# Kernel optimization log

Hardware: AMD Instinct MI355X
Metric: run time of the kernel (lower is better)

## Reference

```python
import jax, jax.numpy as jnp
import numpy as np


def _gcn(x, src, dst, W, b, n):
    # symmetric normalization: deg computed on edges WITH self-loops (weights 1)
    deg = jax.ops.segment_sum(jnp.ones_like(src, dtype=x.dtype), dst, num_segments=n)
    dinv = jnp.where(deg > 0, jax.lax.rsqrt(deg), 0.0)
    norm = dinv[src] * dinv[dst]              # [E+n]
    xw = x @ W                                # [n, out] transform first (cheaper)
    msg = xw[src] * norm[:, None]             # gather + edge scale
    return jax.ops.segment_sum(msg, dst, num_segments=n) + b


def setup_inputs() -> dict:
    key = jax.random.key(0)
    ks = jax.random.split(key, 8)
    N, E = 100_000, 1_280_000
    x = jax.random.normal(ks[0], (N, 18), dtype=jnp.float32)
    edge_index = jax.random.randint(ks[1], (2, E), 0, N, dtype=jnp.int32)
    W1 = jax.random.normal(ks[2], (18, 32), dtype=jnp.float32) * 0.2
    b1 = jnp.zeros((32,), dtype=jnp.float32)
    W2 = jax.random.normal(ks[3], (32, 64), dtype=jnp.float32) * 0.15
    b2 = jnp.zeros((64,), dtype=jnp.float32)
    Wfc = jax.random.normal(ks[4], (64, 2), dtype=jnp.float32) * 0.1
    bfc = jnp.zeros((2,), dtype=jnp.float32)
    return {"x": x, "edge_index": edge_index, "W1": W1, "b1": b1,
            "W2": W2, "b2": b2, "Wfc": Wfc, "bfc": bfc}


def reference(x, edge_index, W1, b1, W2, b2, Wfc, bfc):
    n = x.shape[0]
    loop = jnp.arange(n, dtype=edge_index.dtype)
    src = jnp.concatenate([edge_index[0], loop])   # add self-loops (PyG default)
    dst = jnp.concatenate([edge_index[1], loop])
    h = jax.nn.relu(_gcn(x, src, dst, W1, b1, n))
    h = jax.nn.relu(_gcn(h, src, dst, W2, b2, n))
    logits = h @ Wfc + bfc
    return jax.nn.log_softmax(logits, axis=1)
```

## Files before the change

kernel.cpp:

```cpp
#include <hip/hip_runtime.h>
#include <hip/hip_fp16.h>
#include <math.h>


#define TPB 256
#define BSH 8
#define BNODES 256
#define MAXBUCK 512
#define CH 8192
#define NPW 8
#define CAPSH 13
#define CAP (1 << CAPSH)

__global__ void k_part(const int* __restrict__ src, const int* __restrict__ dst,
                       int* __restrict__ bcursor, int* __restrict__ eb,
                       __half* __restrict__ u1h, __half* __restrict__ u2h,
                       int E, int n, int nbuck) {
    __shared__ int lh[MAXBUCK];
    __shared__ int lbase[MAXBUCK];
    int t = threadIdx.x;
    if (blockIdx.x == 0 && t < 32) {
        u1h[(size_t)n * 32 + t] = __float2half_rn(0.f);
        u2h[(size_t)n * 32 + t] = __float2half_rn(0.f);
    }
    int chunk0 = blockIdx.x * CH;
    int end = min(chunk0 + CH, E);
    const int4* dst4 = (const int4*)dst;
    const int4* src4 = (const int4*)src;
    for (int i = t; i < nbuck; i += TPB) lh[i] = 0;
    __syncthreads();
    for (int e4 = chunk0 / 4 + t; e4 * 4 < end; e4 += TPB) {
        int base = e4 * 4;
        int4 d = dst4[e4];
        if (base + 0 < end) atomicAdd(&lh[d.x >> BSH], 1);
        if (base + 1 < end) atomicAdd(&lh[d.y >> BSH], 1);
        if (base + 2 < end) atomicAdd(&lh[d.z >> BSH], 1);
        if (base + 3 < end) atomicAdd(&lh[d.w >> BSH], 1);
    }
    __syncthreads();
    for (int i = t; i < nbuck; i += TPB) {
        int c = lh[i];
        lbase[i] = c ? atomicAdd(&bcursor[i], c) : 0;
        lh[i] = 0;
    }
    __syncthreads();
    for (int e4 = chunk0 / 4 + t; e4 * 4 < end; e4 += TPB) {
        int base = e4 * 4;
        int4 d = dst4[e4];
        int4 s = src4[e4];
        #define PUT(c, sv) if (base + c < end) { \
            int b = (d.sv) >> BSH; \
            int r = lbase[b] + atomicAdd(&lh[b], 1); \
            if (r < CAP) \
                eb[((size_t)b << CAPSH) + r] = ((s.sv) << BSH) | ((d.sv) & (BNODES - 1)); }
        PUT(0, x) PUT(1, y) PUT(2, z) PUT(3, w)
        #undef PUT
    }
}

__global__ void k_bucket(const int* __restrict__ eb, const int* __restrict__ bcursor,
                         const float* __restrict__ x,
                         int* __restrict__ csr, int* __restrict__ row_start,
                         int* __restrict__ cnt4, float* __restrict__ dinv,
                         __half* __restrict__ u1h, int n) {
    __shared__ int lcnt[BNODES];
    __shared__ int lscan[BNODES];
    __shared__ float ldinv[BNODES];
    int b = blockIdx.x;
    int t = threadIdx.x;
    int node0 = b << BSH;
    int beg = b << CAPSH;
    int end = beg + min(bcursor[b], CAP);
    lcnt[t] = 0;
    __syncthreads();
    for (int i = beg + t; i < end; i += TPB)
        atomicAdd(&lcnt[eb[i] & (BNODES - 1)], 1);
    __syncthreads();
    int v = lcnt[t];
    int pad = (v + 3) & ~3;
    lscan[t] = pad;
    __syncthreads();
    for (int off = 1; off < TPB; off <<= 1) {
        int xx = (t >= off) ? lscan[t - off] : 0;
        __syncthreads();
        lscan[t] += xx;
        __syncthreads();
    }
    int pexcl = lscan[t] - pad;
    int node = node0 + t;
    float dv = rsqrtf(1.0f + (float)v);
    ldinv[t] = dv;
    if (node < n) {
        row_start[node] = beg + pexcl;
        cnt4[node] = pad >> 2;
        dinv[node] = dv;
    }
    __syncthreads();
    lcnt[t] = pexcl;
    __syncthreads();
    for (int i = beg + t; i < end; i += TPB) {
        int e = eb[i];
        int p = atomicAdd(&lcnt[e & (BNODES - 1)], 1);
        csr[beg + p] = e >> BSH;
    }
    __syncthreads();
    for (int p = v; p < pad; ++p) csr[beg + pexcl + p] = n;
    int nn = min(BNODES, n - node0);
    int tot = nn * 32;
    const float* xb = x + (size_t)node0 * 18;
    __half* ub = u1h + (size_t)node0 * 32;
    for (int i = t; i < tot; i += TPB) {
        int nl = i >> 5, f = i & 31;
        float val = (f < 18) ? xb[nl * 18 + f] * ldinv[nl] : 0.f;
        ub[i] = __float2half_rn(val);
    }
}

template <int OS, int NW>
__global__ void k_agg(const __half2* __restrict__ uh2, const int* __restrict__ row_start,
                      const int* __restrict__ cnt4, const int* __restrict__ csr,
                      float* __restrict__ agg, int n) {
    int t = blockIdx.x * blockDim.x + threadIdx.x;
    int node = t >> 4, f2 = t & 15;
    if (node >= n) return;
    int beg = row_start[node];
    int it = cnt4[node];
    float2 acc = __half22float2(uh2[(size_t)node * 16 + f2]);
    const int4* ip = (const int4*)(csr + beg);
    for (int i = 0; i < it; ++i) {
        int4 s = ip[i];
        float2 v0 = __half22float2(uh2[(size_t)s.x * 16 + f2]);
        float2 v1 = __half22float2(uh2[(size_t)s.y * 16 + f2]);
        float2 v2 = __half22float2(uh2[(size_t)s.z * 16 + f2]);
        float2 v3 = __half22float2(uh2[(size_t)s.w * 16 + f2]);
        acc.x += (v0.x + v1.x) + (v2.x + v3.x);
        acc.y += (v0.y + v1.y) + (v2.y + v3.y);
    }
    if (f2 < NW) *(float2*)(agg + (size_t)node * OS + 2 * f2) = acc;
}

__global__ void k_l1(const float* __restrict__ agg1, const float* __restrict__ W1,
                     const float* __restrict__ dinv, const float* __restrict__ b1,
                     __half* __restrict__ u2h, int n) {
    int lane = threadIdx.x & 63;
    int f = lane & 31;
    int wid = __builtin_amdgcn_readfirstlane((int)(threadIdx.x >> 6));
    int wave = blockIdx.x * (TPB / 64) + wid;
    float w1r[18];
#pragma unroll
    for (int k = 0; k < 18; ++k) w1r[k] = W1[k * 32 + f];
    float b1v = b1[f];
    int node0 = wave * NPW;
    for (int r = 0; r < NPW; ++r) {
        int node = node0 + r;
        if (node >= n) return;
        const float* rp = agg1 + (size_t)node * 18;
        float a = 0.f;
#pragma unroll
        for (int k = 0; k < 18; ++k) a = fmaf(rp[k], w1r[k], a);
        float di = dinv[node];
        if (lane < 32)
            u2h[(size_t)node * 32 + f] =
                __float2half_rn(fmaxf(fmaf(di, a, b1v), 0.f) * di);
    }
}

__global__ void k_l2_out(const float* __restrict__ agg2, const float* __restrict__ W2,
                         const float* __restrict__ dinv, const float* __restrict__ b2,
                         const float* __restrict__ Wfc, const float* __restrict__ bfc,
                         float* __restrict__ out, int n) {
    int lane = threadIdx.x & 63;
    int wid = __builtin_amdgcn_readfirstlane((int)(threadIdx.x >> 6));
    int wave = blockIdx.x * (TPB / 64) + wid;
    float w2r[32];
#pragma unroll
    for (int k = 0; k < 32; ++k) w2r[k] = W2[k * 64 + lane];
    float b2v = b2[lane];
    float wf0 = Wfc[lane * 2 + 0], wf1 = Wfc[lane * 2 + 1];
    float bf0 = bfc[0], bf1 = bfc[1];
    int node0 = wave * NPW;
    for (int r = 0; r < NPW; ++r) {
        int node = node0 + r;
        if (node >= n) return;
        const float* rp = agg2 + (size_t)node * 32;
        float a0 = 0.f, a1 = 0.f, a2 = 0.f, a3 = 0.f;
#pragma unroll
        for (int k = 0; k < 32; k += 4) {
            a0 = fmaf(rp[k],     w2r[k],     a0);
            a1 = fmaf(rp[k + 1], w2r[k + 1], a1);
            a2 = fmaf(rp[k + 2], w2r[k + 2], a2);
            a3 = fmaf(rp[k + 3], w2r[k + 3], a3);
        }
        float a = (a0 + a1) + (a2 + a3);
        float v = fmaxf(fmaf(dinv[node], a, b2v), 0.f);
        float l0 = v * wf0;
        float l1 = v * wf1;
#pragma unroll
        for (int off = 32; off >= 1; off >>= 1) {
            l0 += __shfl_xor(l0, off, 64);
            l1 += __shfl_xor(l1, off, 64);
        }
        if (lane == 0) {
            l0 += bf0;
            l1 += bf1;
            float m2 = fmaxf(l0, l1);
            float lse = m2 + logf(expf(l0 - m2) + expf(l1 - m2));
            out[node * 2 + 0] = l0 - lse;
            out[node * 2 + 1] = l1 - lse;
        }
    }
}

extern "C" void kernel_launch(void* const* d_in, const int* in_sizes, int n_in,
                              void* d_out, int out_size, void* d_ws, size_t ws_size,
                              hipStream_t stream) {
    const float* x   = (const float*)d_in[0];
    const int*   ei  = (const int*)d_in[1];
    const float* W1  = (const float*)d_in[2];
    const float* b1  = (const float*)d_in[3];
    const float* W2  = (const float*)d_in[4];
    const float* b2  = (const float*)d_in[5];
    const float* Wfc = (const float*)d_in[6];
    const float* bfc = (const float*)d_in[7];
    float* out = (float*)d_out;

    const int n = in_sizes[0] / 18;
    const int E = in_sizes[1] / 2;
    const int* src = ei;
    const int* dst = ei + E;
    const int nbuck = (n + BNODES - 1) >> BSH;

    char* w = (char*)d_ws;
    int*    bcursor   = (int*)w;     w += (size_t)nbuck * 4;
    int*    row_start = (int*)w;     w += (size_t)n * 4;
    int*    cnt4      = (int*)w;     w += (size_t)n * 4;
    float*  dinv      = (float*)w;   w += (size_t)n * 4;
    int*    eb        = (int*)w;     w += (size_t)nbuck * CAP * 4;
    int*    csr       = (int*)w;     w += (size_t)nbuck * CAP * 4;
    float*  agg1      = (float*)w;   w += (size_t)n * 18 * 4;
    float*  agg2      = (float*)w;   w += (size_t)n * 32 * 4;
    w = (char*)(((size_t)w + 63) & ~(size_t)63);
    __half* u1h       = (__half*)w;  w += (size_t)(n + 1) * 32 * 2;
    w = (char*)(((size_t)w + 63) & ~(size_t)63);
    __half* u2h       = (__half*)w;  w += (size_t)(n + 1) * 32 * 2;

    auto blocks = [](long long work) { return (int)((work + TPB - 1) / TPB); };

    hipMemsetAsync(bcursor, 0, (size_t)nbuck * 4, stream);
    k_part<<<(E + CH - 1) / CH, TPB, 0, stream>>>(src, dst, bcursor, eb, u1h, u2h, E, n, nbuck);
    k_bucket<<<nbuck, TPB, 0, stream>>>(eb, bcursor, x, csr, row_start, cnt4, dinv, u1h, n);

    const int blocksA = blocks((long long)n * 16);
    const int wavesT = (n + NPW - 1) / NPW;
    const int blocksT = (wavesT + (TPB / 64) - 1) / (TPB / 64);

    k_agg<18, 9><<<blocksA, TPB, 0, stream>>>((const __half2*)u1h, row_start, cnt4, csr, agg1, n);
    k_l1<<<blocksT, TPB, 0, stream>>>(agg1, W1, dinv, b1, u2h, n);

    k_agg<32, 16><<<blocksA, TPB, 0, stream>>>((const __half2*)u2h, row_start, cnt4, csr, agg2, n);
    k_l2_out<<<blocksT, TPB, 0, stream>>>(agg2, W2, dinv, b2, Wfc, bfc, out, n);
}
```

Measured before the change: 195.6 us.

## Fuse neighbor aggregation with dense transform via shared-memory staging per wave

Merges each aggregation kernel with its following per-node linear layer, so aggregated features are staged in LDS instead of written to and reread from global agg1/agg2 buffers. The gather now uses 8 lanes per node, each loading 8-byte (four half) chunks instead of 16 lanes with 4-byte loads, and each wave handles 8 nodes. This removes two kernel launches and the intermediate global traffic. In exchange, lanes within a wave may diverge on degree imbalance, and register pressure from the weight arrays in the same kernel may reduce occupancy.

Result: faster. 180.5 us (-7.8%).

```diff
diff --git a/kernel.cpp b/kernel.cpp
--- a/kernel.cpp
+++ b/kernel.cpp
@@ -8,7 +8,6 @@
 #define BNODES 256
 #define MAXBUCK 512
 #define CH 8192
-#define NPW 8
 #define CAPSH 13
 #define CAP (1 << CAPSH)
 
@@ -116,83 +115,132 @@
     }
 }
 
-template <int OS, int NW>
-__global__ void k_agg(const __half2* __restrict__ uh2, const int* __restrict__ row_start,
-                      const int* __restrict__ cnt4, const int* __restrict__ csr,
-                      float* __restrict__ agg, int n) {
-    int t = blockIdx.x * blockDim.x + threadIdx.x;
-    int node = t >> 4, f2 = t & 15;
-    if (node >= n) return;
-    int beg = row_start[node];
-    int it = cnt4[node];
-    float2 acc = __half22float2(uh2[(size_t)node * 16 + f2]);
-    const int4* ip = (const int4*)(csr + beg);
-    for (int i = 0; i < it; ++i) {
-        int4 s = ip[i];
-        float2 v0 = __half22float2(uh2[(size_t)s.x * 16 + f2]);
-        float2 v1 = __half22float2(uh2[(size_t)s.y * 16 + f2]);
-        float2 v2 = __half22float2(uh2[(size_t)s.z * 16 + f2]);
-        float2 v3 = __half22float2(uh2[(size_t)s.w * 16 + f2]);
-        acc.x += (v0.x + v1.x) + (v2.x + v3.x);
-        acc.y += (v0.y + v1.y) + (v2.y + v3.y);
-    }
-    if (f2 < NW) *(float2*)(agg + (size_t)node * OS + 2 * f2) = acc;
-}
-
-__global__ void k_l1(const float* __restrict__ agg1, const float* __restrict__ W1,
-                     const float* __restrict__ dinv, const float* __restrict__ b1,
-                     __half* __restrict__ u2h, int n) {
-    int lane = threadIdx.x & 63;
-    int f = lane & 31;
-    int wid = __builtin_amdgcn_readfirstlane((int)(threadIdx.x >> 6));
-    int wave = blockIdx.x * (TPB / 64) + wid;
+__global__ void k_fused1(const uint2* __restrict__ u1q, const int* __restrict__ row_start,
+                         const int* __restrict__ cnt4, const int* __restrict__ csr,
+                         const float* __restrict__ dinv, const float* __restrict__ W1,
+                         const float* __restrict__ b1, __half* __restrict__ u2h,
+                         int n) {
+    __shared__ float lagg[4][8][33];
+    int t = threadIdx.x;
+    int lane = t & 63, wv = t >> 6;
+    int q = lane & 7, grp = lane >> 3;
+    int f = lane & 31, h = lane >> 5;
     float w1r[18];
 #pragma unroll
     for (int k = 0; k < 18; ++k) w1r[k] = W1[k * 32 + f];
     float b1v = b1[f];
-    int node0 = wave * NPW;
-    for (int r = 0; r < NPW; ++r) {
-        int node = node0 + r;
-        if (node >= n) return;
-        const float* rp = agg1 + (size_t)node * 18;
-        float a = 0.f;
-#pragma unroll
-        for (int k = 0; k < 18; ++k) a = fmaf(rp[k], w1r[k], a);
-        float di = dinv[node];
-        if (lane < 32)
-            u2h[(size_t)node * 32 + f] =
+    int node0 = (blockIdx.x * 4 + wv) * 8;
+    int node = node0 + grp;
+    float a0 = 0.f, a1 = 0.f, a2 = 0.f, a3 = 0.f;
+    if (node < n) {
+        uint2 sv = u1q[(size_t)node * 8 + q];
+        __half2* sh = (__half2*)&sv;
+        float2 s01 = __half22float2(sh[0]), s23 = __half22float2(sh[1]);
+        a0 = s01.x; a1 = s01.y; a2 = s23.x; a3 = s23.y;
+        int beg = row_start[node];
+        int it = cnt4[node];
+        const int4* ip = (const int4*)(csr + beg);
+        for (int i = 0; i < it; ++i) {
+            int4 s = ip[i];
+            uint2 v0 = u1q[(size_t)s.x * 8 + q];
+            uint2 v1 = u1q[(size_t)s.y * 8 + q];
+            uint2 v2 = u1q[(size_t)s.z * 8 + q];
+            uint2 v3 = u1q[(size_t)s.w * 8 + q];
+            __half2* p0 = (__half2*)&v0; __half2* p1 = (__half2*)&v1;
+            __half2* p2 = (__half2*)&v2; __half2* p3 = (__half2*)&v3;
+            float2 f00 = __half22float2(p0[0]), f01 = __half22float2(p0[1]);
+            float2 f10 = __half22float2(p1[0]), f11 = __half22float2(p1[1]);
+            float2 f20 = __half22float2(p2[0]), f21 = __half22float2(p2[1]);
+            float2 f30 = __half22float2(p3[0]), f31 = __half22float2(p3[1]);
+            a0 += (f00.x + f10.x) + (f20.x + f30.x);
+            a1 += (f00.y + f10.y) + (f20.y + f30.y);
+            a2 += (f01.x + f11.x) + (f21.x + f31.x);
+            a3 += (f01.y + f11.y) + (f21.y + f31.y);
+        }
+    }
+    lagg[wv][grp][4 * q + 0] = a0;
+    lagg[wv][grp][4 * q + 1] = a1;
+    lagg[wv][grp][4 * q + 2] = a2;
+    lagg[wv][grp][4 * q + 3] = a3;
+#pragma unroll
+    for (int r = 0; r < 4; ++r) {
+        int nl = 2 * r + h;
+        int nodeT = node0 + nl;
+        if (nodeT < n) {
+            const float* rp = lagg[wv][nl];
+            float a = 0.f;
+#pragma unroll
+            for (int k = 0; k < 18; ++k) a = fmaf(rp[k], w1r[k], a);
+            float di = dinv[nodeT];
+            u2h[(size_t)nodeT * 32 + f] =
                 __float2half_rn(fmaxf(fmaf(di, a, b1v), 0.f) * di);
-    }
-}
-
-__global__ void k_l2_out(const float* __restrict__ agg2, const float* __restrict__ W2,
-                         const float* __restrict__ dinv, const float* __restrict__ b2,
-                         const float* __restrict__ Wfc, const float* __restrict__ bfc,
-                         float* __restrict__ out, int n) {
-    int lane = threadIdx.x & 63;
-    int wid = __builtin_amdgcn_readfirstlane((int)(threadIdx.x >> 6));
-    int wave = blockIdx.x * (TPB / 64) + wid;
+        }
+    }
+}
+
+__global__ void k_fused2(const uint2* __restrict__ u2q, const int* __restrict__ row_start,
+                         const int* __restrict__ cnt4, const int* __restrict__ csr,
+                         const float* __restrict__ dinv, const float* __restrict__ W2,
+                         const float* __restrict__ b2, const float* __restrict__ Wfc,
+                         const float* __restrict__ bfc, float* __restrict__ out,
+                         int n) {
+    __shared__ float lagg[4][8][33];
+    int t = threadIdx.x;
+    int lane = t & 63, wv = t >> 6;
+    int q = lane & 7, grp = lane >> 3;
     float w2r[32];
 #pragma unroll
     for (int k = 0; k < 32; ++k) w2r[k] = W2[k * 64 + lane];
     float b2v = b2[lane];
     float wf0 = Wfc[lane * 2 + 0], wf1 = Wfc[lane * 2 + 1];
     float bf0 = bfc[0], bf1 = bfc[1];
-    int node0 = wave * NPW;
-    for (int r = 0; r < NPW; ++r) {
-        int node = node0 + r;
-        if (node >= n) return;
-        const float* rp = agg2 + (size_t)node * 32;
-        float a0 = 0.f, a1 = 0.f, a2 = 0.f, a3 = 0.f;
+    int node0 = (blockIdx.x * 4 + wv) * 8;
+    int node = node0 + grp;
+    float a0 = 0.f, a1 = 0.f, a2 = 0.f, a3 = 0.f;
+    if (node < n) {
+        uint2 sv = u2q[(size_t)node * 8 + q];
+        __half2* sh = (__half2*)&sv;
+        float2 s01 = __half22float2(sh[0]), s23 = __half22float2(sh[1]);
+        a0 = s01.x; a1 = s01.y; a2 = s23.x; a3 = s23.y;
+        int beg = row_start[node];
+        int it = cnt4[node];
+        const int4* ip = (const int4*)(csr + beg);
+        for (int i = 0; i < it; ++i) {
+            int4 s = ip[i];
+            uint2 v0 = u2q[(size_t)s.x * 8 + q];
+            uint2 v1 = u2q[(size_t)s.y * 8 + q];
+            uint2 v2 = u2q[(size_t)s.z * 8 + q];
+            uint2 v3 = u2q[(size_t)s.w * 8 + q];
+            __half2* p0 = (__half2*)&v0; __half2* p1 = (__half2*)&v1;
+            __half2* p2 = (__half2*)&v2; __half2* p3 = (__half2*)&v3;
+            float2 f00 = __half22float2(p0[0]), f01 = __half22float2(p0[1]);
+            float2 f10 = __half22float2(p1[0]), f11 = __half22float2(p1[1]);
+            float2 f20 = __half22float2(p2[0]), f21 = __half22float2(p2[1]);
+            float2 f30 = __half22float2(p3[0]), f31 = __half22float2(p3[1]);
+            a0 += (f00.x + f10.x) + (f20.x + f30.x);
+            a1 += (f00.y + f10.y) + (f20.y + f30.y);
+            a2 += (f01.x + f11.x) + (f21.x + f31.x);
+            a3 += (f01.y + f11.y) + (f21.y + f31.y);
+        }
+    }
+    lagg[wv][grp][4 * q + 0] = a0;
+    lagg[wv][grp][4 * q + 1] = a1;
+    lagg[wv][grp][4 * q + 2] = a2;
+    lagg[wv][grp][4 * q + 3] = a3;
+#pragma unroll
+    for (int r = 0; r < 8; ++r) {
+        int nodeT = node0 + r;
+        const float* rp = lagg[wv][r];
+        float c0 = 0.f, c1 = 0.f, c2 = 0.f, c3 = 0.f;
 #pragma unroll
         for (int k = 0; k < 32; k += 4) {
-            a0 = fmaf(rp[k],     w2r[k],     a0);
-            a1 = fmaf(rp[k + 1], w2r[k + 1], a1);
-            a2 = fmaf(rp[k + 2], w2r[k + 2], a2);
-            a3 = fmaf(rp[k + 3], w2r[k + 3], a3);
-        }
-        float a = (a0 + a1) + (a2 + a3);
-        float v = fmaxf(fmaf(dinv[node], a, b2v), 0.f);
+            c0 = fmaf(rp[k],     w2r[k],     c0);
+            c1 = fmaf(rp[k + 1], w2r[k + 1], c1);
+            c2 = fmaf(rp[k + 2], w2r[k + 2], c2);
+            c3 = fmaf(rp[k + 3], w2r[k + 3], c3);
+        }
+        float a = (c0 + c1) + (c2 + c3);
+        float v = (nodeT < n) ? fmaxf(fmaf(dinv[nodeT], a, b2v), 0.f) : 0.f;
         float l0 = v * wf0;
         float l1 = v * wf1;
 #pragma unroll
@@ -200,13 +248,13 @@
             l0 += __shfl_xor(l0, off, 64);
             l1 += __shfl_xor(l1, off, 64);
         }
-        if (lane == 0) {
+        if (lane == 0 && nodeT < n) {
             l0 += bf0;
             l1 += bf1;
             float m2 = fmaxf(l0, l1);
             float lse = m2 + logf(expf(l0 - m2) + expf(l1 - m2));
-            out[node * 2 + 0] = l0 - lse;
-            out[node * 2 + 1] = l1 - lse;
+            out[nodeT * 2 + 0] = l0 - lse;
+            out[nodeT * 2 + 1] = l1 - lse;
         }
     }
 }
@@ -237,26 +285,20 @@
     float*  dinv      = (float*)w;   w += (size_t)n * 4;
     int*    eb        = (int*)w;     w += (size_t)nbuck * CAP * 4;
     int*    csr       = (int*)w;     w += (size_t)nbuck * CAP * 4;
-    float*  agg1      = (float*)w;   w += (size_t)n * 18 * 4;
-    float*  agg2      = (float*)w;   w += (size_t)n * 32 * 4;
     w = (char*)(((size_t)w + 63) & ~(size_t)63);
     __half* u1h       = (__half*)w;  w += (size_t)(n + 1) * 32 * 2;
     w = (char*)(((size_t)w + 63) & ~(size_t)63);
     __half* u2h       = (__half*)w;  w += (size_t)(n + 1) * 32 * 2;
 
-    auto blocks = [](long long work) { return (int)((work + TPB - 1) / TPB); };
-
     hipMemsetAsync(bcursor, 0, (size_t)nbuck * 4, stream);
     k_part<<<(E + CH - 1) / CH, TPB, 0, stream>>>(src, dst, bcursor, eb, u1h, u2h, E, n, nbuck);
     k_bucket<<<nbuck, TPB, 0, stream>>>(eb, bcursor, x, csr, row_start, cnt4, dinv, u1h, n);
 
-    const int blocksA = blocks((long long)n * 16);
-    const int wavesT = (n + NPW - 1) / NPW;
-    const int blocksT = (wavesT + (TPB / 64) - 1) / (TPB / 64);
-
-    k_agg<18, 9><<<blocksA, TPB, 0, stream>>>((const __half2*)u1h, row_start, cnt4, csr, agg1, n);
-    k_l1<<<blocksT, TPB, 0, stream>>>(agg1, W1, dinv, b1, u2h, n);
-
-    k_agg<32, 16><<<blocksA, TPB, 0, stream>>>((const __half2*)u2h, row_start, cnt4, csr, agg2, n);
-    k_l2_out<<<blocksT, TPB, 0, stream>>>(agg2, W2, dinv, b2, Wfc, bfc, out, n);
-}
+    const int waves = (n + 7) / 8;
+    const int blocksF = (waves + 3) / 4;
+
+    k_fused1<<<blocksF, TPB, 0, stream>>>((const uint2*)u1h, row_start, cnt4, csr,
+                                          dinv, W1, b1, u2h, n);
+    k_fused2<<<blocksF, TPB, 0, stream>>>((const uint2*)u2h, row_start, cnt4, csr,
+                                          dinv, W2, b2, Wfc, bfc, out, n);
+}
```
